# Performance work log

Measured on AMD Instinct MI355X. Metric: run time of the kernel, lower is better.

The kernel has to match this reference:

```python
import jax, jax.numpy as jnp
import numpy as np

N_ACTIVE = 200000
C = 64
N_ROWS = 524288  # B*L original (batch, length) sites


def setup_inputs() -> dict:
    key = jax.random.key(0)
    k1, k2 = jax.random.split(key)
    features = jax.random.normal(k1, (N_ACTIVE, C), dtype=jnp.float32)
    rules = jax.random.randint(k2, (N_ROWS,), 0, N_ACTIVE, dtype=jnp.int64)
    return {"features": features, "rules": rules}


def reference(features, rules):
    # BLOutputLayer forward: rule-book gather from sparse active-site
    # features [nActive, C] back to original BL row order [B*L, C].
    return jnp.take(features, rules, axis=0)
```

## Files before the change

### kernel.cpp

```cpp
#include <hip/hip_runtime.h>
#include <hip/hip_bf16.h>


#define C_FLOAT4 16
#define ROWS_PER_BLOCK 16

__global__ __launch_bounds__(256) void BLOutputLayer_gather_kernel(
    const float4* __restrict__ features,
    const int* __restrict__ rules,
    float4* __restrict__ out,
    int n_rows) {
    const int tid  = threadIdx.x;
    const int lane = tid & (C_FLOAT4 - 1);
    const int row  = blockIdx.x * ROWS_PER_BLOCK + (tid >> 4);
    if (row >= n_rows) return;

    const int src = rules[row];
    out[(size_t)row * C_FLOAT4 + lane] = features[(size_t)src * C_FLOAT4 + lane];
}

extern "C" void kernel_launch(void* const* d_in, const int* in_sizes, int n_in,
                              void* d_out, int out_size, void* d_ws, size_t ws_size,
                              hipStream_t stream) {
    const float4* features = (const float4*)d_in[0];
    const int*    rules    = (const int*)d_in[1];
    float4*       out      = (float4*)d_out;

    const int n_rows = in_sizes[1];
    const int grid   = (n_rows + ROWS_PER_BLOCK - 1) / ROWS_PER_BLOCK;

    BLOutputLayer_gather_kernel<<<grid, 256, 0, stream>>>(features, rules, out, n_rows);
}
```

Baseline: 184.6 us.

## Batch 16 gathered rows per thread with LDS-staged rules and nontemporal stores

Each block now handles 256 rows. Their rule indices are staged in LDS with one coalesced load, and each thread then issues 16 independent 16-byte feature loads before storing them with nontemporal stores. The aim is more memory-level parallelism per thread, less launch and indexing overhead per row, and less cache pollution from the streamed output. In exchange the grid is 16x smaller and each thread needs more registers, which could lower occupancy.

```diff
diff --git a/kernel.cpp b/kernel.cpp
--- a/kernel.cpp
+++ b/kernel.cpp
@@ -2,32 +2,68 @@
 #include <hip/hip_bf16.h>
 
 
-#define C_FLOAT4 16
-#define ROWS_PER_BLOCK 16
+typedef float f4 __attribute__((ext_vector_type(4)));
 
-__global__ __launch_bounds__(256) void BLOutputLayer_gather_kernel(
-    const float4* __restrict__ features,
+#define BLOCK 256
+#define ROWS_PER_BLOCK 256
+#define C_F4 16
+#define ROWS_PER_THREAD 16
+
+__global__ __launch_bounds__(BLOCK) void BLOutputLayer_gather_kernel(
+    const f4* __restrict__ features,
     const int* __restrict__ rules,
-    float4* __restrict__ out,
+    f4* __restrict__ out,
     int n_rows) {
-    const int tid  = threadIdx.x;
-    const int lane = tid & (C_FLOAT4 - 1);
-    const int row  = blockIdx.x * ROWS_PER_BLOCK + (tid >> 4);
-    if (row >= n_rows) return;
+    __shared__ int lds_rules[ROWS_PER_BLOCK];
 
-    const int src = rules[row];
-    out[(size_t)row * C_FLOAT4 + lane] = features[(size_t)src * C_FLOAT4 + lane];
+    const int t    = threadIdx.x;
+    const int base = blockIdx.x * ROWS_PER_BLOCK;
+
+    {
+        const int r = base + t;
+        lds_rules[t] = (r < n_rows) ? rules[r] : 0;
+    }
+    __syncthreads();
+
+    const int lane = t & (C_F4 - 1);
+    const int g    = t >> 4;
+
+    if (base + ROWS_PER_BLOCK <= n_rows) {
+        int src[ROWS_PER_THREAD];
+#pragma unroll
+        for (int j = 0; j < ROWS_PER_THREAD; ++j)
+            src[j] = lds_rules[g + C_F4 * j];
+
+        f4 v[ROWS_PER_THREAD];
+#pragma unroll
+        for (int j = 0; j < ROWS_PER_THREAD; ++j)
+            v[j] = features[(size_t)src[j] * C_F4 + lane];
+
+#pragma unroll
+        for (int j = 0; j < ROWS_PER_THREAD; ++j) {
+            const int row = base + g + C_F4 * j;
+            __builtin_nontemporal_store(v[j], &out[(size_t)row * C_F4 + lane]);
+        }
+    } else {
+        for (int j = 0; j < ROWS_PER_THREAD; ++j) {
+            const int row = base + g + C_F4 * j;
+            if (row < n_rows) {
+                const int s = lds_rules[g + C_F4 * j];
+                out[(size_t)row * C_F4 + lane] = features[(size_t)s * C_F4 + lane];
+            }
+        }
+    }
 }
 
 extern "C" void kernel_launch(void* const* d_in, const int* in_sizes, int n_in,
                               void* d_out, int out_size, void* d_ws, size_t ws_size,
                               hipStream_t stream) {
-    const float4* features = (const float4*)d_in[0];
-    const int*    rules    = (const int*)d_in[1];
-    float4*       out      = (float4*)d_out;
+    const f4*  features = (const f4*)d_in[0];
+    const int* rules    = (const int*)d_in[1];
+    f4*        out      = (f4*)d_out;
 
     const int n_rows = in_sizes[1];
     const int grid   = (n_rows + ROWS_PER_BLOCK - 1) / ROWS_PER_BLOCK;
 
-    BLOutputLayer_gather_kernel<<<grid, 256, 0, stream>>>(features, rules, out, n_rows);
+    BLOutputLayer_gather_kernel<<<grid, BLOCK, 0, stream>>>(features, rules, out, n_rows);
 }
```

After: 182.7 us. About the same (-1.1%).
